# Kernel optimization log

Measured on AMD Instinct MI355X. Metric: run time of the kernel, lower is better.

The kernel has to match this reference:

```python
import jax, jax.numpy as jnp
import numpy as np

IGNORE = 0  # ignore label (default in LovaszSoftmax.__init__)


def setup_inputs() -> dict:
    key = jax.random.key(0)
    k1, k2 = jax.random.split(key)
    B, C, H, W = 4, 20, 512, 1024
    logits = jax.random.normal(k1, (B, C, H, W), dtype=jnp.float32)
    labels = jax.random.randint(k2, (B, H, W), 0, 20, dtype=jnp.int32)
    return {"logits": logits, "labels": labels}


def _lovasz_softmax(logits, labels, ignore=IGNORE):
    # logits: [B,C,H,W], labels: [B,H,W]
    B, C, H, W = logits.shape
    probas = jax.nn.softmax(logits, axis=1)
    pf = probas.transpose(0, 2, 3, 1).reshape(-1, C)  # [N, C]
    lf = labels.reshape(-1)                            # [N]
    valid = lf != ignore                               # [N]

    def per_class(c):
        # Ignored pixels get fg=0 and pred=0 -> error 0, so they sort to the
        # tail and contribute 0 to the dot product (equivalent to filtering
        # them out, but jit-compatible with static shapes).
        fg = ((lf == c) & valid).astype(pf.dtype)      # [N]
        pred = jnp.where(valid, pf[:, c], 0.0)         # [N]
        errors = jnp.abs(fg - pred)
        order = jnp.argsort(-errors)                   # descending sort perm
        errors_sorted = errors[order]
        fg_sorted = fg[order]
        # Lovasz gradient of sorted ground truth
        gts = fg_sorted.sum()
        intersection = gts - jnp.cumsum(fg_sorted)
        union = gts + jnp.cumsum(1.0 - fg_sorted)
        jaccard = 1.0 - intersection / union
        jaccard = jnp.concatenate([jaccard[:1], jaccard[1:] - jaccard[:-1]])
        loss_c = jnp.dot(errors_sorted, jaccard)
        present = fg.sum() > 0                          # classes='present'
        return loss_c, present

    losses, present = jax.vmap(per_class)(jnp.arange(C))
    p = present.astype(losses.dtype)
    # mean over present classes (matches 'present' + mean() in torch source)
    return jnp.sum(losses * p) / jnp.maximum(jnp.sum(p), 1.0)


def reference(logits, labels):
    return _lovasz_softmax(logits, labels, IGNORE)
```

## Files before the change

### kernel.cpp

```cpp
#include <hip/hip_runtime.h>

#define NCLS 20
#define NBIN 512
#define BATCH 4
#define HWSZ (512*1024)
#define NPIX (BATCH*HWSZ)

__global__ void hist_kernel(const float* __restrict__ logits,
                            const int* __restrict__ labels,
                            unsigned long long* __restrict__ ghist)
{
    __shared__ unsigned int lh[NCLS * NBIN];
    for (int i = threadIdx.x; i < NCLS * NBIN; i += blockDim.x) lh[i] = 0u;
    __syncthreads();

    const int tid = blockIdx.x * blockDim.x + threadIdx.x;
    const int nthreads = gridDim.x * blockDim.x;

    for (int n = tid; n < NPIX; n += nthreads) {
        const int b  = n >> 19;
        const int hw = n & (HWSZ - 1);
        const float* base = logits + (size_t)b * NCLS * HWSZ + hw;

        float x[NCLS];
        float m = -1e30f;
#pragma unroll
        for (int c = 0; c < NCLS; c++) {
            x[c] = base[(size_t)c * HWSZ];
            m = fmaxf(m, x[c]);
        }
        float Z = 0.f;
#pragma unroll
        for (int c = 0; c < NCLS; c++) {
            x[c] = __expf(x[c] - m);
            Z += x[c];
        }
        const float invZ = 1.f / Z;

        const int lbl = labels[n];
        const bool valid = (lbl != 0);

#pragma unroll
        for (int c = 0; c < NCLS; c++) {
            const float p = x[c] * invZ;
            const bool fg = valid && (lbl == c);
            const float e = valid ? (fg ? 1.f - p : p) : 0.f;
            int bin = (int)(e * (float)NBIN);
            bin = bin > (NBIN - 1) ? (NBIN - 1) : bin;
            atomicAdd(&lh[c * NBIN + bin], fg ? 0x10001u : 1u);
        }
    }
    __syncthreads();

    for (int i = threadIdx.x; i < NCLS * NBIN; i += blockDim.x) {
        const unsigned v = lh[i];
        if (v) {
            unsigned long long add =
                (unsigned long long)(v & 0xFFFFu) |
                ((unsigned long long)(v >> 16) << 32);
            atomicAdd(&ghist[i], add);
        }
    }
}

__global__ void scan_kernel(const unsigned long long* __restrict__ ghist,
                            float* __restrict__ cls)
{
    const int c = blockIdx.x;
    const int lane = threadIdx.x;
    const unsigned long long* h = ghist + c * NBIN;

    unsigned fgsum = 0;
    for (int j = lane; j < NBIN; j += 64)
        fgsum += (unsigned)(h[j] >> 32);
    for (int off = 32; off; off >>= 1)
        fgsum += __shfl_down(fgsum, off);
    const unsigned gts = __shfl(fgsum, 0);

    float loss = 0.f;
    if (gts > 0) {
        const float fgts = (float)gts;
        unsigned Tc = 0, Fc = 0;
        float acc = 0.f;
        for (int chunk = 0; chunk < NBIN / 64; chunk++) {
            const int k = NBIN - 1 - (chunk * 64 + lane);
            const unsigned long long v = h[k];
            const unsigned cnt = (unsigned)(v & 0xFFFFFFFFull);
            const unsigned fg  = (unsigned)(v >> 32);

            unsigned ci = cnt, fi = fg;
            for (int off = 1; off < 64; off <<= 1) {
                const unsigned cu = __shfl_up(ci, off);
                const unsigned fu = __shfl_up(fi, off);
                if (lane >= off) { ci += cu; fi += fu; }
            }
            const unsigned T1 = Tc + ci, F1 = Fc + fi;
            const unsigned T0 = T1 - cnt, F0 = F1 - fg;

            const float J1 = 1.f - (fgts - (float)F1) /
                                   (fgts + (float)T1 - (float)F1);
            const float J0 = 1.f - (fgts - (float)F0) /
                                   (fgts + (float)T0 - (float)F0);
            const float center = ((float)k + 0.5f) * (1.0f / (float)NBIN);
            acc += center * (J1 - J0);

            Tc = __shfl(T1, 63);
            Fc = __shfl(F1, 63);
        }
        for (int off = 32; off; off >>= 1)
            acc += __shfl_down(acc, off);
        loss = acc;
    }
    if (lane == 0) {
        cls[c]        = loss;
        cls[NCLS + c] = (gts > 0) ? 1.f : 0.f;
    }
}

__global__ void finalize_kernel(const float* __restrict__ cls,
                                float* __restrict__ out)
{
    if (threadIdx.x == 0 && blockIdx.x == 0) {
        float sl = 0.f, sp = 0.f;
        for (int c = 0; c < NCLS; c++) {
            sl += cls[c] * cls[NCLS + c];
            sp += cls[NCLS + c];
        }
        out[0] = sl / fmaxf(sp, 1.f);
    }
}

extern "C" void kernel_launch(void* const* d_in, const int* in_sizes, int n_in,
                              void* d_out, int out_size, void* d_ws, size_t ws_size,
                              hipStream_t stream)
{
    const float* logits = (const float*)d_in[0];
    const int*   labels = (const int*)d_in[1];

    unsigned long long* ghist = (unsigned long long*)d_ws;
    float* cls = (float*)((char*)d_ws + (size_t)NCLS * NBIN * 8);

    hipMemsetAsync(d_ws, 0, (size_t)NCLS * NBIN * 8 + 2 * NCLS * 4, stream);

    hist_kernel<<<512, 1024, 0, stream>>>(logits, labels, ghist);
    scan_kernel<<<NCLS, 64, 0, stream>>>(ghist, cls);
    finalize_kernel<<<1, 1, 0, stream>>>(cls, (float*)d_out);
}
```

Measured before the change: 264.2 us.

## Replicate shared histograms and write per-block partials instead of global atomics

Cuts the histogram bins from 512 to 192 and keeps four interleaved copies of the shared-memory histogram, selected by thread index, to spread LDS atomic contention. Each block now writes its partial histogram to global memory with plain stores, which removes the global 64-bit atomics and the memset. The scan kernel then sums the 512 per-block partials for each bin. Fewer bins make the error quantisation coarser, which may affect accuracy, and the packed 16-bit counters per block still risk overflow.

```diff
diff --git a/kernel.cpp b/kernel.cpp
--- a/kernel.cpp
+++ b/kernel.cpp
@@ -1,23 +1,26 @@
 #include <hip/hip_runtime.h>
 
 #define NCLS 20
-#define NBIN 512
-#define BATCH 4
+#define NBIN 192
+#define RREP 4
 #define HWSZ (512*1024)
-#define NPIX (BATCH*HWSZ)
+#define NPIX (4*HWSZ)
+#define NBLK 512
+#define NTHR 1024
 
-__global__ void hist_kernel(const float* __restrict__ logits,
-                            const int* __restrict__ labels,
-                            unsigned long long* __restrict__ ghist)
+__global__ __launch_bounds__(NTHR)
+void hist_kernel(const float* __restrict__ logits,
+                 const int* __restrict__ labels,
+                 unsigned int* __restrict__ bhist)
 {
-    __shared__ unsigned int lh[NCLS * NBIN];
-    for (int i = threadIdx.x; i < NCLS * NBIN; i += blockDim.x) lh[i] = 0u;
+    __shared__ unsigned int lh[NCLS * NBIN * RREP];
+    for (int i = threadIdx.x; i < NCLS * NBIN * RREP; i += NTHR) lh[i] = 0u;
     __syncthreads();
 
-    const int tid = blockIdx.x * blockDim.x + threadIdx.x;
-    const int nthreads = gridDim.x * blockDim.x;
+    const int tid = blockIdx.x * NTHR + threadIdx.x;
+    const int r = threadIdx.x & (RREP - 1);
 
-    for (int n = tid; n < NPIX; n += nthreads) {
+    for (int n = tid; n < NPIX; n += NBLK * NTHR) {
         const int b  = n >> 19;
         const int hw = n & (HWSZ - 1);
         const float* base = logits + (size_t)b * NCLS * HWSZ + hw;
@@ -47,73 +50,75 @@
             const float e = valid ? (fg ? 1.f - p : p) : 0.f;
             int bin = (int)(e * (float)NBIN);
             bin = bin > (NBIN - 1) ? (NBIN - 1) : bin;
-            atomicAdd(&lh[c * NBIN + bin], fg ? 0x10001u : 1u);
+            atomicAdd(&lh[(c * NBIN + bin) * RREP + r], fg ? 0x10001u : 1u);
         }
     }
     __syncthreads();
 
-    for (int i = threadIdx.x; i < NCLS * NBIN; i += blockDim.x) {
-        const unsigned v = lh[i];
-        if (v) {
-            unsigned long long add =
-                (unsigned long long)(v & 0xFFFFu) |
-                ((unsigned long long)(v >> 16) << 32);
-            atomicAdd(&ghist[i], add);
-        }
+    unsigned int* out = bhist + (size_t)blockIdx.x * (NCLS * NBIN);
+    for (int i = threadIdx.x; i < NCLS * NBIN; i += NTHR) {
+        out[i] = lh[i * RREP + 0] + lh[i * RREP + 1] +
+                 lh[i * RREP + 2] + lh[i * RREP + 3];
     }
 }
 
-__global__ void scan_kernel(const unsigned long long* __restrict__ ghist,
+__global__ void scan_kernel(const unsigned int* __restrict__ bhist,
                             float* __restrict__ cls)
 {
+    __shared__ float scnt[NBIN];
+    __shared__ float sfg[NBIN];
     const int c = blockIdx.x;
-    const int lane = threadIdx.x;
-    const unsigned long long* h = ghist + c * NBIN;
+    const int t = threadIdx.x;
 
-    unsigned fgsum = 0;
-    for (int j = lane; j < NBIN; j += 64)
-        fgsum += (unsigned)(h[j] >> 32);
-    for (int off = 32; off; off >>= 1)
-        fgsum += __shfl_down(fgsum, off);
-    const unsigned gts = __shfl(fgsum, 0);
+    unsigned int cnt = 0, fg = 0;
+    for (int b = 0; b < NBLK; b++) {
+        const unsigned int v = bhist[(size_t)b * (NCLS * NBIN) + c * NBIN + t];
+        cnt += v & 0xFFFFu;
+        fg  += v >> 16;
+    }
+    scnt[t] = (float)cnt;
+    sfg[t]  = (float)fg;
+    __syncthreads();
 
-    float loss = 0.f;
-    if (gts > 0) {
-        const float fgts = (float)gts;
-        unsigned Tc = 0, Fc = 0;
-        float acc = 0.f;
-        for (int chunk = 0; chunk < NBIN / 64; chunk++) {
-            const int k = NBIN - 1 - (chunk * 64 + lane);
-            const unsigned long long v = h[k];
-            const unsigned cnt = (unsigned)(v & 0xFFFFFFFFull);
-            const unsigned fg  = (unsigned)(v >> 32);
+    if (t < 64) {
+        const int lane = t;
+        float fgsum = 0.f;
+        for (int j = lane; j < NBIN; j += 64) fgsum += sfg[j];
+        for (int off = 32; off; off >>= 1) fgsum += __shfl_down(fgsum, off);
+        const float gts = __shfl(fgsum, 0);
 
-            unsigned ci = cnt, fi = fg;
-            for (int off = 1; off < 64; off <<= 1) {
-                const unsigned cu = __shfl_up(ci, off);
-                const unsigned fu = __shfl_up(fi, off);
-                if (lane >= off) { ci += cu; fi += fu; }
+        float loss = 0.f;
+        if (gts > 0.f) {
+            float Tc = 0.f, Fc = 0.f;
+            float acc = 0.f;
+            for (int chunk = 0; chunk < NBIN / 64; chunk++) {
+                const int k = NBIN - 1 - (chunk * 64 + lane);
+                float ci = scnt[k];
+                float fi = sfg[k];
+                const float cnt_k = ci, fg_k = fi;
+                for (int off = 1; off < 64; off <<= 1) {
+                    const float cu = __shfl_up(ci, off);
+                    const float fu = __shfl_up(fi, off);
+                    if (lane >= off) { ci += cu; fi += fu; }
+                }
+                const float T1 = Tc + ci, F1 = Fc + fi;
+                const float T0 = T1 - cnt_k, F0 = F1 - fg_k;
+
+                const float J1 = 1.f - (gts - F1) / (gts + T1 - F1);
+                const float J0 = 1.f - (gts - F0) / (gts + T0 - F0);
+                const float center = ((float)k + 0.5f) * (1.0f / (float)NBIN);
+                acc += center * (J1 - J0);
+
+                Tc = __shfl(T1, 63);
+                Fc = __shfl(F1, 63);
             }
-            const unsigned T1 = Tc + ci, F1 = Fc + fi;
-            const unsigned T0 = T1 - cnt, F0 = F1 - fg;
-
-            const float J1 = 1.f - (fgts - (float)F1) /
-                                   (fgts + (float)T1 - (float)F1);
-            const float J0 = 1.f - (fgts - (float)F0) /
-                                   (fgts + (float)T0 - (float)F0);
-            const float center = ((float)k + 0.5f) * (1.0f / (float)NBIN);
-            acc += center * (J1 - J0);
-
-            Tc = __shfl(T1, 63);
-            Fc = __shfl(F1, 63);
+            for (int off = 32; off; off >>= 1) acc += __shfl_down(acc, off);
+            loss = acc;
         }
-        for (int off = 32; off; off >>= 1)
-            acc += __shfl_down(acc, off);
-        loss = acc;
-    }
-    if (lane == 0) {
-        cls[c]        = loss;
-        cls[NCLS + c] = (gts > 0) ? 1.f : 0.f;
+        if (lane == 0) {
+            cls[c]        = loss;
+            cls[NCLS + c] = (gts > 0.f) ? 1.f : 0.f;
+        }
     }
 }
 
@@ -137,12 +142,10 @@
     const float* logits = (const float*)d_in[0];
     const int*   labels = (const int*)d_in[1];
 
-    unsigned long long* ghist = (unsigned long long*)d_ws;
-    float* cls = (float*)((char*)d_ws + (size_t)NCLS * NBIN * 8);
+    unsigned int* bhist = (unsigned int*)d_ws;
+    float* cls = (float*)((char*)d_ws + (size_t)NBLK * NCLS * NBIN * 4);
 
-    hipMemsetAsync(d_ws, 0, (size_t)NCLS * NBIN * 8 + 2 * NCLS * 4, stream);
-
-    hist_kernel<<<512, 1024, 0, stream>>>(logits, labels, ghist);
-    scan_kernel<<<NCLS, 64, 0, stream>>>(ghist, cls);
+    hist_kernel<<<NBLK, NTHR, 0, stream>>>(logits, labels, bhist);
+    scan_kernel<<<NCLS, NBIN, 0, stream>>>(bhist, cls);
     finalize_kernel<<<1, 1, 0, stream>>>(cls, (float*)d_out);
 }
```

After: 266.0 us. Within noise of the previous version (+0.7%).
